# Optimization experiments

Measured on AMD Instinct MI355X. Metric: run time of the kernel, lower is better.

Reference implementation:

```python
import jax, jax.numpy as jnp
import numpy as np

B, S, CL = 64, 250, 16
WV, CV, FV, LAB = 50000, 100, 10, 20
WD, CD, CH, FD, HD = 300, 300, 50, 5, 200
T = LAB + 2          # CRF lattice size (labels + START + STOP)
START, STOP = LAB, LAB + 1
H = HD // 2          # hidden per LSTM direction
IN = CH + WD + FD    # 355


def _lstm_dir(x, m, w_ih, w_hh, b):
    # x: [B,S,IN], m: [B,S] bool -> masked unidirectional LSTM (PyTorch gate order i,f,g,o)
    Bn = x.shape[0]
    def step(carry, inp):
        h, c = carry
        xt, mt = inp
        g = xt @ w_ih.T + h @ w_hh.T + b
        i, f, gg, o = jnp.split(g, 4, axis=-1)
        c_new = jax.nn.sigmoid(f) * c + jax.nn.sigmoid(i) * jnp.tanh(gg)
        h_new = jax.nn.sigmoid(o) * jnp.tanh(c_new)
        mt = mt[:, None]
        h = jnp.where(mt, h_new, h)
        c = jnp.where(mt, c_new, c)
        return (h, c), h
    init = (jnp.zeros((Bn, H), x.dtype), jnp.zeros((Bn, H), x.dtype))
    _, hs = jax.lax.scan(step, init, (x.transpose(1, 0, 2), m.T))
    return hs.transpose(1, 0, 2)  # [B,S,H]


def _viterbi(feats, mask, trans):
    # feats: [B,S,T], mask: [B,S] bool, trans: [T,T] (trans[i,j] = score i->j)
    Bn = feats.shape[0]
    delta0 = trans[START][None, :] + feats[:, 0]  # [B,T]
    ident = jnp.arange(T)[None, :]
    def step(delta, inp):
        f_t, m_t = inp                              # [B,T], [B]
        sc = delta[:, :, None] + trans[None]        # [B,T(prev),T(cur)]
        vmax = sc.max(axis=1)
        bp = sc.argmax(axis=1)                      # [B,T]
        m = m_t[:, None]
        delta = jnp.where(m, vmax + f_t, delta)
        bp = jnp.where(m, bp, ident)                # pads: pass-through pointer
        return delta, bp
    delta, bps = jax.lax.scan(step, delta0,
                              (feats[:, 1:].transpose(1, 0, 2), mask[:, 1:].T))
    final = delta + trans[:, STOP][None, :]
    score = final.max(axis=1)                       # [B]
    last = final.argmax(axis=1)                     # [B]
    ar = jnp.arange(Bn)
    def back(tag, bp):
        prev = bp[ar, tag]
        return prev, prev
    _, prevs = jax.lax.scan(back, last, bps, reverse=True)  # [S-1,B]
    tag_seq = jnp.concatenate([prevs.transpose(1, 0), last[:, None]], axis=1)  # [B,S]
    return score, tag_seq


def setup_inputs() -> dict:
    key = jax.random.key(0)
    ks = jax.random.split(key, 20)
    lens = jax.random.randint(ks[0], (B,), S // 2, S + 1)
    mask = (jnp.arange(S)[None, :] < lens[:, None])
    def u(k, shape, scale):
        return jax.random.uniform(k, shape, jnp.float32, -scale, scale)
    return {
        "batch_word": jax.random.randint(ks[1], (B, S), 0, WV),
        "batch_features": jax.random.randint(ks[2], (B, S), 0, FV),
        "batch_wordlen": lens,
        "batch_char": jax.random.randint(ks[3], (B * S, CL), 0, CV),
        "batch_charlen": jax.random.randint(ks[4], (B * S,), 1, CL + 1),
        "batch_charrecover": jnp.arange(B * S),
        "mask": mask,
        "char_emb": u(ks[5], (CV, CD), np.sqrt(3.0 / CD)),
        "word_emb": u(ks[6], (WV, WD), np.sqrt(3.0 / WD)),
        "feat_emb": u(ks[7], (FV, FD), np.sqrt(3.0 / FD)),
        "conv_w": 0.1 * jax.random.normal(ks[8], (CH, CD, 3), jnp.float32),
        "conv_b": jnp.zeros((CH,), jnp.float32),
        "w_ih_f": 0.1 * jax.random.normal(ks[9], (4 * H, IN), jnp.float32),
        "w_hh_f": 0.1 * jax.random.normal(ks[10], (4 * H, H), jnp.float32),
        "b_f": jnp.zeros((4 * H,), jnp.float32),
        "w_ih_b": 0.1 * jax.random.normal(ks[11], (4 * H, IN), jnp.float32),
        "w_hh_b": 0.1 * jax.random.normal(ks[12], (4 * H, H), jnp.float32),
        "b_b": jnp.zeros((4 * H,), jnp.float32),
        "proj_w": 0.1 * jax.random.normal(ks[13], (HD, T), jnp.float32),
        "proj_b": jnp.zeros((T,), jnp.float32),
        "trans": 0.1 * jax.random.normal(ks[14], (T, T), jnp.float32),
    }


def reference(batch_word, batch_features, batch_wordlen, batch_char, batch_charlen,
              batch_charrecover, mask, char_emb, word_emb, feat_emb, conv_w, conv_b,
              w_ih_f, w_hh_f, b_f, w_ih_b, w_hh_b, b_b, proj_w, proj_b, trans):
    # char CNN: embed -> conv1d(k=3, pad=1) -> global max-pool (dropout: eval mode, identity)
    ce = char_emb[batch_char]                          # [B*S, CL, CD]
    conv = jax.lax.conv_general_dilated(
        ce.transpose(0, 2, 1), conv_w, window_strides=(1,), padding=[(1, 1)],
        dimension_numbers=('NCH', 'OIH', 'NCH')) + conv_b[None, :, None]
    char_feat = conv.max(axis=2)                       # [B*S, CH]
    char_feat = char_feat[batch_charrecover].reshape(B, S, CH)
    word_rep = jnp.concatenate(
        [word_emb[batch_word], char_feat, feat_emb[batch_features]], axis=2)  # [B,S,IN]
    # masked BiLSTM (equivalent to pack_padded_sequence: pads never update state)
    h_f = _lstm_dir(word_rep, mask, w_ih_f, w_hh_f, b_f)
    h_b = _lstm_dir(word_rep[:, ::-1], mask[:, ::-1], w_ih_b, w_hh_b, b_b)[:, ::-1]
    lstm_out = jnp.concatenate([h_f, h_b], axis=2)     # [B,S,HD]
    feats = lstm_out @ proj_w + proj_b                 # [B,S,T]
    score, tag_seq = _viterbi(feats, mask, trans)
    return tag_seq
```

## Files before the change

kernel.cpp:

```cpp
#include <hip/hip_runtime.h>
#include <hip/hip_bf16.h>
#include <math.h>

#define WS_U        0
#define WS_WPAD     15360
#define WS_WREP     359424
#define WS_PRE      6503424
#define WS_LSTM     359424
#define WS_FEATS    3559424

__global__ __launch_bounds__(256) void prepw_kernel(
    const float* __restrict__ wf, const float* __restrict__ wb,
    float* __restrict__ w_pad) {
  int idx = blockIdx.x * 256 + threadIdx.x;
  if (idx >= 896 * 384) return;
  int col = idx % 384, row = idx / 384;
  float v = 0.f;
  if (col < 355) {
    if (row < 400)      v = wf[row * 355 + col];
    else if (row < 800) v = wb[(row - 400) * 355 + col];
  }
  w_pad[idx] = v;
}

__global__ __launch_bounds__(256) void u_kernel(
    const float* __restrict__ char_emb, const float* __restrict__ conv_w,
    float* __restrict__ U) {
  int idx = blockIdx.x * 256 + threadIdx.x;
  if (idx >= 15000) return;
  int c = idx / 150, rem = idx % 150, k = rem / 50, o = rem % 50;
  float acc = 0.f;
  for (int i = 0; i < 300; i++)
    acc += char_emb[c * 300 + i] * conv_w[(o * 300 + i) * 3 + k];
  U[idx] = acc;
}

__global__ __launch_bounds__(64) void assemble_kernel(
    const int* __restrict__ batch_word, const int* __restrict__ batch_feats,
    const int* __restrict__ batch_char, const int* __restrict__ recover,
    const float* __restrict__ word_emb, const float* __restrict__ feat_emb,
    const float* __restrict__ conv_b, const float* __restrict__ U,
    float* __restrict__ wrep) {
  int n = blockIdx.x;
  int tid = threadIdx.x;
  __shared__ int ch[16];
  if (tid < 16) ch[tid] = batch_char[(size_t)recover[n] * 16 + tid];
  __syncthreads();
  float* dst = wrep + (size_t)n * 384;
  int w = batch_word[n];
  for (int i = tid; i < 300; i += 64) dst[i] = word_emb[(size_t)w * 300 + i];
  if (tid < 34) {
    int i = 350 + tid;
    dst[i] = (i < 355) ? feat_emb[batch_feats[n] * 5 + (i - 350)] : 0.f;
  }
  if (tid < 50) {
    int o = tid;
    float bo = conv_b[o];
    float m = -1e30f;
#pragma unroll
    for (int l = 0; l < 16; l++) {
      float v = bo + U[(ch[l] * 3 + 1) * 50 + o];
      if (l > 0)  v += U[(ch[l - 1] * 3 + 0) * 50 + o];
      if (l < 15) v += U[(ch[l + 1] * 3 + 2) * 50 + o];
      m = fmaxf(m, v);
    }
    dst[300 + o] = m;
  }
}

__global__ __launch_bounds__(256, 4) void gemm_kernel(
    const float* __restrict__ A, const float* __restrict__ B,
    float* __restrict__ C, const float* __restrict__ bf,
    const float* __restrict__ bb) {
  __shared__ float As[16][128];
  __shared__ float Bs[16][128];
  int tid = threadIdx.x;
  int m0 = blockIdx.x * 128;
  int n0 = blockIdx.y * 128;
  int tx = tid & 15, ty = tid >> 4;
  int lr = tid >> 2;
  int lc = (tid & 3) * 4;
  float acc[8][8];
#pragma unroll
  for (int i = 0; i < 8; i++)
#pragma unroll
    for (int j = 0; j < 8; j++) acc[i][j] = 0.f;

  for (int k0 = 0; k0 < 384; k0 += 16) {
#pragma unroll
    for (int h = 0; h < 2; h++) {
      int row = lr + h * 64;
      float4 av = *(const float4*)(A + (size_t)(m0 + row) * 384 + k0 + lc);
      As[lc + 0][row] = av.x; As[lc + 1][row] = av.y;
      As[lc + 2][row] = av.z; As[lc + 3][row] = av.w;
      float4 bv = *(const float4*)(B + (size_t)(n0 + row) * 384 + k0 + lc);
      Bs[lc + 0][row] = bv.x; Bs[lc + 1][row] = bv.y;
      Bs[lc + 2][row] = bv.z; Bs[lc + 3][row] = bv.w;
    }
    __syncthreads();
#pragma unroll
    for (int k = 0; k < 16; k++) {
      float a[8], b[8];
      *(float4*)&a[0] = *(const float4*)&As[k][ty * 8];
      *(float4*)&a[4] = *(const float4*)&As[k][ty * 8 + 4];
      *(float4*)&b[0] = *(const float4*)&Bs[k][tx * 8];
      *(float4*)&b[4] = *(const float4*)&Bs[k][tx * 8 + 4];
#pragma unroll
      for (int i = 0; i < 8; i++)
#pragma unroll
        for (int j = 0; j < 8; j++) acc[i][j] += a[i] * b[j];
    }
    __syncthreads();
  }
#pragma unroll
  for (int i = 0; i < 8; i++) {
    int m = m0 + ty * 8 + i;
#pragma unroll
    for (int jj = 0; jj < 8; jj++) {
      int j = n0 + tx * 8 + jj;
      if (j < 800) {
        float bias = (j < 400) ? bf[j] : bb[j - 400];
        C[(size_t)m * 800 + j] = acc[i][jj] + bias;
      }
    }
  }
}

__global__ __launch_bounds__(256, 2) void lstm_kernel(
    const float* __restrict__ pre, const float* __restrict__ w_hh_f,
    const float* __restrict__ w_hh_b, const int* __restrict__ wordlen,
    float* __restrict__ lstm_out) {
  int tid = threadIdx.x;
  int dir = blockIdx.x >> 6;
  int r = blockIdx.x & 63;
  int len = wordlen[r];
  const float* __restrict__ Wh = dir ? w_hh_b : w_hh_f;
  __shared__ float h_sh[128];
  __shared__ float g_sh[400];
  float W1[100], W2[100];
  int j1 = tid, j2 = tid + 200;
  if (tid < 200) {
    const float4* w1 = (const float4*)(Wh + j1 * 100);
    const float4* w2 = (const float4*)(Wh + j2 * 100);
#pragma unroll
    for (int q = 0; q < 25; q++) {
      float4 a = w1[q], b = w2[q];
      W1[4 * q] = a.x; W1[4 * q + 1] = a.y; W1[4 * q + 2] = a.z; W1[4 * q + 3] = a.w;
      W2[4 * q] = b.x; W2[4 * q + 1] = b.y; W2[4 * q + 2] = b.z; W2[4 * q + 3] = b.w;
    }
  }
  if (tid < 128) h_sh[tid] = 0.f;
  float c_reg = 0.f;
  const float* __restrict__ pr = pre + dir * 400;
  int p0 = dir ? 249 : 0;
  int dp = dir ? -1 : 1;
  size_t rowbase = (size_t)r * 250;
  float pv1 = 0.f, pv2 = 0.f;
  if (tid < 200) {
    size_t off = (rowbase + p0) * 800;
    pv1 = pr[off + j1];
    pv2 = pr[off + j2];
  }
  __syncthreads();
  for (int i = 0; i < 250; i++) {
    int p = p0 + dp * i;
    if (tid < 200) {
      float g1 = pv1, g2 = pv2;
      if (i < 249) {
        size_t off = (rowbase + p + dp) * 800;
        pv1 = pr[off + j1];
        pv2 = pr[off + j2];
      }
#pragma unroll
      for (int q = 0; q < 25; q++) {
        float4 hv = *(const float4*)&h_sh[4 * q];
        g1 += hv.x * W1[4 * q]     + hv.y * W1[4 * q + 1]
            + hv.z * W1[4 * q + 2] + hv.w * W1[4 * q + 3];
        g2 += hv.x * W2[4 * q]     + hv.y * W2[4 * q + 1]
            + hv.z * W2[4 * q + 2] + hv.w * W2[4 * q + 3];
      }
      g_sh[j1] = g1;
      g_sh[j2] = g2;
    }
    __syncthreads();
    if (tid < 100) {
      float gi = g_sh[tid], gf = g_sh[100 + tid];
      float gg = g_sh[200 + tid], go = g_sh[300 + tid];
      float hv;
      if (p < len) {
        float si = 1.f / (1.f + expf(-gi));
        float sf = 1.f / (1.f + expf(-gf));
        float so = 1.f / (1.f + expf(-go));
        c_reg = sf * c_reg + si * tanhf(gg);
        hv = so * tanhf(c_reg);
        h_sh[tid] = hv;
      } else {
        hv = h_sh[tid];
      }
      lstm_out[(rowbase + p) * 200 + dir * 100 + tid] = hv;
    }
    __syncthreads();
  }
}

__global__ __launch_bounds__(256) void proj_kernel(
    const float* __restrict__ lstm_out, const float* __restrict__ proj_w,
    const float* __restrict__ proj_b, float* __restrict__ feats) {
  __shared__ float L[8][200];
  int tid = threadIdx.x;
  size_t base = (size_t)blockIdx.x * 8 * 200;
  for (int idx = tid; idx < 1600; idx += 256)
    L[idx / 200][idx % 200] = lstm_out[base + idx];
  __syncthreads();
  int ty = tid >> 5, c = tid & 31;
  if (c < 22) {
    float acc = proj_b[c];
#pragma unroll 8
    for (int k = 0; k < 200; k++) acc += L[ty][k] * proj_w[k * 22 + c];
    feats[((size_t)blockIdx.x * 8 + ty) * 22 + c] = acc;
  }
}

__global__ __launch_bounds__(64) void viterbi_kernel(
    const float* __restrict__ feats, const float* __restrict__ trans,
    const int* __restrict__ wordlen, int* __restrict__ out) {
  int r = blockIdx.x;
  int lane = threadIdx.x;
  __shared__ float dsh[22];
  __shared__ float tsh[22][23];
  __shared__ unsigned char bps[250][22];
  int len = wordlen[r];
  const float* __restrict__ fr = feats + (size_t)r * 250 * 22;
  for (int idx = lane; idx < 484; idx += 64)
    tsh[idx / 22][idx % 22] = trans[idx];
  if (lane < 22) dsh[lane] = trans[20 * 22 + lane] + fr[lane];
  __syncthreads();
  for (int t = 1; t < 250; t++) {
    float best = -1e30f, fv = 0.f;
    int arg = 0;
    if (lane < 22) {
      fv = fr[t * 22 + lane];
#pragma unroll
      for (int k = 0; k < 22; k++) {
        float cand = dsh[k] + tsh[k][lane];
        if (cand > best) { best = cand; arg = k; }
      }
    }
    __syncthreads();
    if (lane < 22) {
      bool valid = t < len;
      if (valid) dsh[lane] = best + fv;
      bps[t][lane] = valid ? (unsigned char)arg : (unsigned char)lane;
    }
    __syncthreads();
  }
  if (lane == 0) {
    float best = -1e30f;
    int last = 0;
#pragma unroll
    for (int k = 0; k < 22; k++) {
      float cand = dsh[k] + tsh[k][21];
      if (cand > best) { best = cand; last = k; }
    }
    int tag = last;
    out[r * 250 + 249] = tag;
    for (int t = 249; t >= 1; t--) {
      tag = bps[t][tag];
      out[r * 250 + t - 1] = tag;
    }
  }
}

extern "C" void kernel_launch(void* const* d_in, const int* in_sizes, int n_in,
                              void* d_out, int out_size, void* d_ws, size_t ws_size,
                              hipStream_t stream) {
  const int* batch_word  = (const int*)d_in[0];
  const int* batch_feats = (const int*)d_in[1];
  const int* wordlen     = (const int*)d_in[2];
  const int* batch_char  = (const int*)d_in[3];
  const int* recover     = (const int*)d_in[5];
  const float* char_emb  = (const float*)d_in[7];
  const float* word_emb  = (const float*)d_in[8];
  const float* feat_emb  = (const float*)d_in[9];
  const float* conv_w    = (const float*)d_in[10];
  const float* conv_b    = (const float*)d_in[11];
  const float* w_ih_f    = (const float*)d_in[12];
  const float* w_hh_f    = (const float*)d_in[13];
  const float* b_f       = (const float*)d_in[14];
  const float* w_ih_b    = (const float*)d_in[15];
  const float* w_hh_b    = (const float*)d_in[16];
  const float* b_b       = (const float*)d_in[17];
  const float* proj_w    = (const float*)d_in[18];
  const float* proj_b    = (const float*)d_in[19];
  const float* trans     = (const float*)d_in[20];
  int* out = (int*)d_out;
  float* ws = (float*)d_ws;

  float* U        = ws + WS_U;
  float* w_pad    = ws + WS_WPAD;
  float* wrep     = ws + WS_WREP;
  float* pre      = ws + WS_PRE;
  float* lstm_out = ws + WS_LSTM;
  float* feats    = ws + WS_FEATS;

  prepw_kernel<<<1344, 256, 0, stream>>>(w_ih_f, w_ih_b, w_pad);
  u_kernel<<<59, 256, 0, stream>>>(char_emb, conv_w, U);
  assemble_kernel<<<16000, 64, 0, stream>>>(batch_word, batch_feats, batch_char,
                                            recover, word_emb, feat_emb, conv_b,
                                            U, wrep);
  dim3 ggrid(125, 7);
  gemm_kernel<<<ggrid, 256, 0, stream>>>(wrep, w_pad, pre, b_f, b_b);
  lstm_kernel<<<128, 256, 0, stream>>>(pre, w_hh_f, w_hh_b, wordlen, lstm_out);
  proj_kernel<<<2000, 256, 0, stream>>>(lstm_out, proj_w, proj_b, feats);
  viterbi_kernel<<<64, 64, 0, stream>>>(feats, trans, wordlen, out);
}
```

Baseline: 793.7 us.

## Replace LSTM barriers with atomic counter sync and per-wave redundant h update

The LSTM kernel now runs 8 waves, each owning 50 gate rows, and swaps the two __syncthreads per step for a workgroup-scope atomic counter plus spin wait. Gate sums are double-buffered, and every wave recomputes the full cell update into its own private h copy, so no second barrier is needed. Pre-activations are prefetched two steps ahead. The Viterbi kernel preloads its feats row into shared memory and double-buffers delta, cutting one barrier per step. The trade-off is redundant transcendental work in every wave, plus spin-wait costs and reliance on wave progress guarantees for correctness.

```diff
diff --git a/kernel.cpp b/kernel.cpp
--- a/kernel.cpp
+++ b/kernel.cpp
@@ -126,80 +126,96 @@
   }
 }
 
-__global__ __launch_bounds__(256, 2) void lstm_kernel(
+__global__ __launch_bounds__(512) void lstm_kernel(
     const float* __restrict__ pre, const float* __restrict__ w_hh_f,
     const float* __restrict__ w_hh_b, const int* __restrict__ wordlen,
     float* __restrict__ lstm_out) {
   int tid = threadIdx.x;
+  int w = tid >> 6, l = tid & 63;
   int dir = blockIdx.x >> 6;
   int r = blockIdx.x & 63;
   int len = wordlen[r];
   const float* __restrict__ Wh = dir ? w_hh_b : w_hh_f;
-  __shared__ float h_sh[128];
-  __shared__ float g_sh[400];
-  float W1[100], W2[100];
-  int j1 = tid, j2 = tid + 200;
-  if (tid < 200) {
-    const float4* w1 = (const float4*)(Wh + j1 * 100);
-    const float4* w2 = (const float4*)(Wh + j2 * 100);
+
+  __shared__ float gbuf[2][400];
+  __shared__ float hbuf[8][100];
+  __shared__ int cnt;
+
+  bool act = (l < 50);
+  int j = 50 * w + l;
+
+  float W[100];
+  if (act) {
+    const float4* wp = (const float4*)(Wh + (size_t)j * 100);
 #pragma unroll
     for (int q = 0; q < 25; q++) {
-      float4 a = w1[q], b = w2[q];
-      W1[4 * q] = a.x; W1[4 * q + 1] = a.y; W1[4 * q + 2] = a.z; W1[4 * q + 3] = a.w;
-      W2[4 * q] = b.x; W2[4 * q + 1] = b.y; W2[4 * q + 2] = b.z; W2[4 * q + 3] = b.w;
-    }
-  }
-  if (tid < 128) h_sh[tid] = 0.f;
-  float c_reg = 0.f;
+      float4 t = wp[q];
+      W[4 * q] = t.x; W[4 * q + 1] = t.y; W[4 * q + 2] = t.z; W[4 * q + 3] = t.w;
+    }
+  }
+  float c1 = 0.f, c2 = 0.f, h1 = 0.f, h2 = 0.f;
+
+  if (tid == 0) cnt = 0;
+  for (int idx = tid; idx < 800; idx += 512) ((float*)hbuf)[idx] = 0.f;
+  __syncthreads();
+
   const float* __restrict__ pr = pre + dir * 400;
   int p0 = dir ? 249 : 0;
   int dp = dir ? -1 : 1;
   size_t rowbase = (size_t)r * 250;
-  float pv1 = 0.f, pv2 = 0.f;
-  if (tid < 200) {
-    size_t off = (rowbase + p0) * 800;
-    pv1 = pr[off + j1];
-    pv2 = pr[off + j2];
-  }
-  __syncthreads();
+
+  float pvA = 0.f, pvB = 0.f;
+  if (act) {
+    pvA = pr[(rowbase + p0) * 800 + j];
+    pvB = pr[(rowbase + p0 + dp) * 800 + j];
+  }
+
   for (int i = 0; i < 250; i++) {
     int p = p0 + dp * i;
-    if (tid < 200) {
-      float g1 = pv1, g2 = pv2;
-      if (i < 249) {
-        size_t off = (rowbase + p + dp) * 800;
-        pv1 = pr[off + j1];
-        pv2 = pr[off + j2];
-      }
+    int ph = i & 1;
+    if (act) {
+      float g = pvA;
+      pvA = pvB;
+      if (i + 2 < 250)
+        pvB = pr[(rowbase + p + 2 * dp) * 800 + j];
+      const float4* hb = (const float4*)hbuf[w];
 #pragma unroll
       for (int q = 0; q < 25; q++) {
-        float4 hv = *(const float4*)&h_sh[4 * q];
-        g1 += hv.x * W1[4 * q]     + hv.y * W1[4 * q + 1]
-            + hv.z * W1[4 * q + 2] + hv.w * W1[4 * q + 3];
-        g2 += hv.x * W2[4 * q]     + hv.y * W2[4 * q + 1]
-            + hv.z * W2[4 * q + 2] + hv.w * W2[4 * q + 3];
-      }
-      g_sh[j1] = g1;
-      g_sh[j2] = g2;
-    }
-    __syncthreads();
-    if (tid < 100) {
-      float gi = g_sh[tid], gf = g_sh[100 + tid];
-      float gg = g_sh[200 + tid], go = g_sh[300 + tid];
-      float hv;
+        float4 hv = hb[q];
+        g += hv.x * W[4 * q]     + hv.y * W[4 * q + 1]
+           + hv.z * W[4 * q + 2] + hv.w * W[4 * q + 3];
+      }
+      gbuf[ph][j] = g;
+    }
+    if (l == 0)
+      __hip_atomic_fetch_add(&cnt, 1, __ATOMIC_RELEASE, __HIP_MEMORY_SCOPE_WORKGROUP);
+    int tgt = 8 * (i + 1);
+    while (__hip_atomic_load(&cnt, __ATOMIC_ACQUIRE, __HIP_MEMORY_SCOPE_WORKGROUP) < tgt) {}
+    if (act) {
+      float gi1 = gbuf[ph][l],      gf1 = gbuf[ph][100 + l];
+      float gg1 = gbuf[ph][200 + l], go1 = gbuf[ph][300 + l];
+      float gi2 = gbuf[ph][50 + l],  gf2 = gbuf[ph][150 + l];
+      float gg2 = gbuf[ph][250 + l], go2 = gbuf[ph][350 + l];
       if (p < len) {
-        float si = 1.f / (1.f + expf(-gi));
-        float sf = 1.f / (1.f + expf(-gf));
-        float so = 1.f / (1.f + expf(-go));
-        c_reg = sf * c_reg + si * tanhf(gg);
-        hv = so * tanhf(c_reg);
-        h_sh[tid] = hv;
-      } else {
-        hv = h_sh[tid];
-      }
-      lstm_out[(rowbase + p) * 200 + dir * 100 + tid] = hv;
-    }
-    __syncthreads();
+        float si1 = 1.f / (1.f + expf(-gi1));
+        float sf1 = 1.f / (1.f + expf(-gf1));
+        float so1 = 1.f / (1.f + expf(-go1));
+        c1 = sf1 * c1 + si1 * tanhf(gg1);
+        h1 = so1 * tanhf(c1);
+        float si2 = 1.f / (1.f + expf(-gi2));
+        float sf2 = 1.f / (1.f + expf(-gf2));
+        float so2 = 1.f / (1.f + expf(-go2));
+        c2 = sf2 * c2 + si2 * tanhf(gg2);
+        h2 = so2 * tanhf(c2);
+      }
+      hbuf[w][l] = h1;
+      hbuf[w][50 + l] = h2;
+      if (w == 0) {
+        float* o = lstm_out + (rowbase + p) * 200 + dir * 100;
+        o[l] = h1;
+        o[50 + l] = h2;
+      }
+    }
   }
 }
 
@@ -226,30 +242,31 @@
     const int* __restrict__ wordlen, int* __restrict__ out) {
   int r = blockIdx.x;
   int lane = threadIdx.x;
-  __shared__ float dsh[22];
+  __shared__ float fsh[5500];
   __shared__ float tsh[22][23];
+  __shared__ float dsh[2][22];
   __shared__ unsigned char bps[250][22];
   int len = wordlen[r];
-  const float* __restrict__ fr = feats + (size_t)r * 250 * 22;
+  const float* __restrict__ fr = feats + (size_t)r * 5500;
+  for (int idx = lane; idx < 5500; idx += 64) fsh[idx] = fr[idx];
   for (int idx = lane; idx < 484; idx += 64)
     tsh[idx / 22][idx % 22] = trans[idx];
-  if (lane < 22) dsh[lane] = trans[20 * 22 + lane] + fr[lane];
+  __syncthreads();
+  if (lane < 22) dsh[0][lane] = tsh[20][lane] + fsh[lane];
   __syncthreads();
   for (int t = 1; t < 250; t++) {
-    float best = -1e30f, fv = 0.f;
-    int arg = 0;
+    int ph = t & 1;
     if (lane < 22) {
-      fv = fr[t * 22 + lane];
+      float fv = fsh[t * 22 + lane];
+      float best = -1e30f;
+      int arg = 0;
 #pragma unroll
       for (int k = 0; k < 22; k++) {
-        float cand = dsh[k] + tsh[k][lane];
+        float cand = dsh[1 - ph][k] + tsh[k][lane];
         if (cand > best) { best = cand; arg = k; }
       }
-    }
-    __syncthreads();
-    if (lane < 22) {
       bool valid = t < len;
-      if (valid) dsh[lane] = best + fv;
+      dsh[ph][lane] = valid ? (best + fv) : dsh[1 - ph][lane];
       bps[t][lane] = valid ? (unsigned char)arg : (unsigned char)lane;
     }
     __syncthreads();
@@ -259,7 +276,7 @@
     int last = 0;
 #pragma unroll
     for (int k = 0; k < 22; k++) {
-      float cand = dsh[k] + tsh[k][21];
+      float cand = dsh[249 & 1][k] + tsh[k][21];
       if (cand > best) { best = cand; last = k; }
     }
     int tag = last;
@@ -310,7 +327,7 @@
                                             U, wrep);
   dim3 ggrid(125, 7);
   gemm_kernel<<<ggrid, 256, 0, stream>>>(wrep, w_pad, pre, b_f, b_b);
-  lstm_kernel<<<128, 256, 0, stream>>>(pre, w_hh_f, w_hh_b, wordlen, lstm_out);
+  lstm_kernel<<<128, 512, 0, stream>>>(pre, w_hh_f, w_hh_b, wordlen, lstm_out);
   proj_kernel<<<2000, 256, 0, stream>>>(lstm_out, proj_w, proj_b, feats);
   viterbi_kernel<<<64, 64, 0, stream>>>(feats, trans, wordlen, out);
 }
```

After: 879.9 us. +10.9%, slower.

## Replace LSTM barriers with LDS counter spin-sync; double-buffer Viterbi state

Applied to the files above, without the earlier changes.

In the LSTM recurrence, the two __syncthreads per step become a workgroup-scope atomic counter. One lane per wavefront increments it and all threads spin with s_sleep until the expected count is reached. The launch-bounds occupancy hint is also removed. Viterbi preloads the row's feats into LDS and double-buffers delta, cutting one barrier per step, and the GEMM LDS tiles are padded to avoid bank conflicts. Spin-waiting may cost more than hardware barriers, and dropping the occupancy hint changes register allocation.

```diff
diff --git a/kernel.cpp b/kernel.cpp
--- a/kernel.cpp
+++ b/kernel.cpp
@@ -72,8 +72,8 @@
     const float* __restrict__ A, const float* __restrict__ B,
     float* __restrict__ C, const float* __restrict__ bf,
     const float* __restrict__ bb) {
-  __shared__ float As[16][128];
-  __shared__ float Bs[16][128];
+  __shared__ float As[16][132];
+  __shared__ float Bs[16][132];
   int tid = threadIdx.x;
   int m0 = blockIdx.x * 128;
   int n0 = blockIdx.y * 128;
@@ -126,7 +126,7 @@
   }
 }
 
-__global__ __launch_bounds__(256, 2) void lstm_kernel(
+__global__ __launch_bounds__(256) void lstm_kernel(
     const float* __restrict__ pre, const float* __restrict__ w_hh_f,
     const float* __restrict__ w_hh_b, const int* __restrict__ wordlen,
     float* __restrict__ lstm_out) {
@@ -135,13 +135,15 @@
   int r = blockIdx.x & 63;
   int len = wordlen[r];
   const float* __restrict__ Wh = dir ? w_hh_b : w_hh_f;
-  __shared__ float h_sh[128];
+  __shared__ __align__(16) float h_sh[100];
   __shared__ float g_sh[400];
+  __shared__ int cnt;
   float W1[100], W2[100];
   int j1 = tid, j2 = tid + 200;
-  if (tid < 200) {
-    const float4* w1 = (const float4*)(Wh + j1 * 100);
-    const float4* w2 = (const float4*)(Wh + j2 * 100);
+  bool dotth = (tid < 200);
+  if (dotth) {
+    const float4* w1 = (const float4*)(Wh + (size_t)j1 * 100);
+    const float4* w2 = (const float4*)(Wh + (size_t)j2 * 100);
 #pragma unroll
     for (int q = 0; q < 25; q++) {
       float4 a = w1[q], b = w2[q];
@@ -149,31 +151,36 @@
       W2[4 * q] = b.x; W2[4 * q + 1] = b.y; W2[4 * q + 2] = b.z; W2[4 * q + 3] = b.w;
     }
   }
-  if (tid < 128) h_sh[tid] = 0.f;
   float c_reg = 0.f;
+  if (tid < 100) h_sh[tid] = 0.f;
+  if (tid == 0) cnt = 0;
+  __syncthreads();
+
   const float* __restrict__ pr = pre + dir * 400;
   int p0 = dir ? 249 : 0;
   int dp = dir ? -1 : 1;
   size_t rowbase = (size_t)r * 250;
+
   float pv1 = 0.f, pv2 = 0.f;
-  if (tid < 200) {
+  if (dotth) {
     size_t off = (rowbase + p0) * 800;
     pv1 = pr[off + j1];
     pv2 = pr[off + j2];
   }
-  __syncthreads();
+
   for (int i = 0; i < 250; i++) {
     int p = p0 + dp * i;
-    if (tid < 200) {
+    if (dotth) {
       float g1 = pv1, g2 = pv2;
       if (i < 249) {
         size_t off = (rowbase + p + dp) * 800;
         pv1 = pr[off + j1];
         pv2 = pr[off + j2];
       }
+      const float4* hb = (const float4*)h_sh;
 #pragma unroll
       for (int q = 0; q < 25; q++) {
-        float4 hv = *(const float4*)&h_sh[4 * q];
+        float4 hv = hb[q];
         g1 += hv.x * W1[4 * q]     + hv.y * W1[4 * q + 1]
             + hv.z * W1[4 * q + 2] + hv.w * W1[4 * q + 3];
         g2 += hv.x * W2[4 * q]     + hv.y * W2[4 * q + 1]
@@ -182,9 +189,12 @@
       g_sh[j1] = g1;
       g_sh[j2] = g2;
     }
-    __syncthreads();
+    if ((tid & 63) == 0)
+      __hip_atomic_fetch_add(&cnt, 1, __ATOMIC_RELEASE, __HIP_MEMORY_SCOPE_WORKGROUP);
+    while (__hip_atomic_load(&cnt, __ATOMIC_ACQUIRE, __HIP_MEMORY_SCOPE_WORKGROUP) < 8 * i + 4)
+      __builtin_amdgcn_s_sleep(1);
     if (tid < 100) {
-      float gi = g_sh[tid], gf = g_sh[100 + tid];
+      float gi = g_sh[tid],       gf = g_sh[100 + tid];
       float gg = g_sh[200 + tid], go = g_sh[300 + tid];
       float hv;
       if (p < len) {
@@ -193,13 +203,16 @@
         float so = 1.f / (1.f + expf(-go));
         c_reg = sf * c_reg + si * tanhf(gg);
         hv = so * tanhf(c_reg);
-        h_sh[tid] = hv;
       } else {
         hv = h_sh[tid];
       }
+      h_sh[tid] = hv;
       lstm_out[(rowbase + p) * 200 + dir * 100 + tid] = hv;
     }
-    __syncthreads();
+    if ((tid & 63) == 0)
+      __hip_atomic_fetch_add(&cnt, 1, __ATOMIC_RELEASE, __HIP_MEMORY_SCOPE_WORKGROUP);
+    while (__hip_atomic_load(&cnt, __ATOMIC_ACQUIRE, __HIP_MEMORY_SCOPE_WORKGROUP) < 8 * i + 8)
+      __builtin_amdgcn_s_sleep(1);
   }
 }
 
@@ -226,30 +239,31 @@
     const int* __restrict__ wordlen, int* __restrict__ out) {
   int r = blockIdx.x;
   int lane = threadIdx.x;
-  __shared__ float dsh[22];
+  __shared__ float fsh[5500];
   __shared__ float tsh[22][23];
+  __shared__ float dsh[2][22];
   __shared__ unsigned char bps[250][22];
   int len = wordlen[r];
-  const float* __restrict__ fr = feats + (size_t)r * 250 * 22;
+  const float* __restrict__ fr = feats + (size_t)r * 5500;
+  for (int idx = lane; idx < 5500; idx += 64) fsh[idx] = fr[idx];
   for (int idx = lane; idx < 484; idx += 64)
     tsh[idx / 22][idx % 22] = trans[idx];
-  if (lane < 22) dsh[lane] = trans[20 * 22 + lane] + fr[lane];
+  __syncthreads();
+  if (lane < 22) dsh[0][lane] = tsh[20][lane] + fsh[lane];
   __syncthreads();
   for (int t = 1; t < 250; t++) {
-    float best = -1e30f, fv = 0.f;
-    int arg = 0;
+    int ph = t & 1;
     if (lane < 22) {
-      fv = fr[t * 22 + lane];
+      float fv = fsh[t * 22 + lane];
+      float best = -1e30f;
+      int arg = 0;
 #pragma unroll
       for (int k = 0; k < 22; k++) {
-        float cand = dsh[k] + tsh[k][lane];
+        float cand = dsh[1 - ph][k] + tsh[k][lane];
         if (cand > best) { best = cand; arg = k; }
       }
-    }
-    __syncthreads();
-    if (lane < 22) {
       bool valid = t < len;
-      if (valid) dsh[lane] = best + fv;
+      dsh[ph][lane] = valid ? (best + fv) : dsh[1 - ph][lane];
       bps[t][lane] = valid ? (unsigned char)arg : (unsigned char)lane;
     }
     __syncthreads();
@@ -259,7 +273,7 @@
     int last = 0;
 #pragma unroll
     for (int k = 0; k < 22; k++) {
-      float cand = dsh[k] + tsh[k][21];
+      float cand = dsh[249 & 1][k] + tsh[k][21];
       if (cand > best) { best = cand; last = k; }
     }
     int tag = last;
```

New measurement: 857.2 us. 8.0% more time.
